# Optimization experiments

Measured on AMD Instinct MI355X. Metric: run time of the kernel, lower is better.

The kernel has to match this reference:

```python
import jax, jax.numpy as jnp
import numpy as np
import math

HEAD_DIM = 32
N_Q_HEADS = 32
N_KV_HEADS = 8
ROPE_BASE = 10000.0
NEG_INF = -1e9


def _rope_cos_sin(seq_len, dtype):
    inv_freq = 1.0 / (ROPE_BASE ** (jnp.arange(0, HEAD_DIM, 2, dtype=jnp.float32) / HEAD_DIM))
    pos = jnp.arange(seq_len, dtype=jnp.float32)
    freqs = pos[:, None] * inv_freq[None, :]          # [S, D/2]
    emb = jnp.concatenate([freqs, freqs], axis=-1)     # [S, D]
    return jnp.cos(emb).astype(dtype), jnp.sin(emb).astype(dtype)


def _rotate_half(x):
    x1, x2 = jnp.split(x, 2, axis=-1)
    return jnp.concatenate([-x2, x1], axis=-1)


def _apply_rope(x, cos, sin):
    # x: [B, H, S, D]; cos/sin: [S, D]
    return x * cos[None, None] + _rotate_half(x) * sin[None, None]


def setup_inputs() -> dict:
    key = jax.random.key(0)
    ks = jax.random.split(key, 5)
    B, S, D = 2, 2048, 1024
    sc = 1.0 / math.sqrt(D)
    return {
        "hidden_states": jax.random.normal(ks[0], (B, S, D), jnp.float32),
        "attention_mask": jnp.ones((B, S), jnp.int32),
        "Wq": jax.random.normal(ks[1], (1024, 1024), jnp.float32) * sc,
        "Wk": jax.random.normal(ks[2], (256, 1024), jnp.float32) * sc,
        "Wv": jax.random.normal(ks[3], (256, 1024), jnp.float32) * sc,
        "Wo": jax.random.normal(ks[4], (1024, 1024), jnp.float32) * sc,
    }


def reference(hidden_states, attention_mask, Wq, Wk, Wv, Wo):
    B, S, D = hidden_states.shape
    group = N_Q_HEADS // N_KV_HEADS

    q = (hidden_states @ Wq.T).reshape(B, S, N_Q_HEADS, HEAD_DIM).transpose(0, 2, 1, 3)
    k = (hidden_states @ Wk.T).reshape(B, S, N_KV_HEADS, HEAD_DIM).transpose(0, 2, 1, 3)
    v = (hidden_states @ Wv.T).reshape(B, S, N_KV_HEADS, HEAD_DIM).transpose(0, 2, 1, 3)

    cos, sin = _rope_cos_sin(S, q.dtype)
    q = _apply_rope(q, cos, sin)
    k = _apply_rope(k, cos, sin)

    k = jnp.repeat(k, group, axis=1)  # [B, 32, S, D]
    v = jnp.repeat(v, group, axis=1)

    scores = jnp.einsum("bhqd,bhkd->bhqk", q, k) / math.sqrt(HEAD_DIM)

    causal = jnp.tril(jnp.ones((S, S), bool))
    allowed = causal[None, None] & (attention_mask[:, None, None, :] != 0)
    scores = jnp.where(allowed, scores, NEG_INF)

    attn = jax.nn.softmax(scores, axis=-1)
    out = jnp.einsum("bhqk,bhkd->bhqd", attn, v)  # [B, 32, S, 32]
    out = out.transpose(0, 2, 1, 3).reshape(B, S, D)
    return out @ Wo.T
```

## Files before the change

kernel.cpp:

```cpp
#include <hip/hip_runtime.h>

typedef __bf16 bf16x8 __attribute__((ext_vector_type(8)));
typedef __bf16 bf16x4 __attribute__((ext_vector_type(4)));
typedef short short4v __attribute__((ext_vector_type(4)));
typedef float f32x4 __attribute__((ext_vector_type(4)));

__device__ __forceinline__ f32x4 mfma16(bf16x8 a, bf16x8 b, f32x4 c) {
  return __builtin_amdgcn_mfma_f32_16x16x32_bf16(a, b, c, 0, 0, 0);
}

__device__ __forceinline__ f32x4 mfma16k16(bf16x4 a, bf16x4 b, f32x4 c) {
#if __has_builtin(__builtin_amdgcn_mfma_f32_16x16x16bf16_1k)
  short4v as = __builtin_bit_cast(short4v, a);
  short4v bs = __builtin_bit_cast(short4v, b);
  return __builtin_amdgcn_mfma_f32_16x16x16bf16_1k(as, bs, c, 0, 0, 0);
#else
  f32x4 d;
  asm volatile("v_mfma_f32_16x16x16_bf16 %0, %1, %2, %3"
               : "=v"(d)
               : "v"(a), "v"(b), "v"(c));
  return d;
#endif
}

__device__ __forceinline__ float fast_exp2(float x) {
  return __builtin_amdgcn_exp2f(x);
}

typedef const __attribute__((address_space(1))) void gvoid_t;
typedef __attribute__((address_space(3))) void svoid_t;
__device__ __forceinline__ void lds16(const __bf16* g, __bf16* l) {
  __builtin_amdgcn_global_load_lds((gvoid_t*)g, (svoid_t*)l, 16, 0, 0);
}

__global__ __launch_bounds__(256) void prep(const float* __restrict__ hidden,
                                            const float* __restrict__ Wq,
                                            const float* __restrict__ Wk,
                                            const float* __restrict__ Wv,
                                            const float* __restrict__ Wo,
                                            __bf16* __restrict__ hb,
                                            __bf16* __restrict__ Wqkvb,
                                            __bf16* __restrict__ Wob) {
  int q = blockIdx.x * 256 + threadIdx.x;
  const float* src;
  __bf16* dst;
  if (q < 1048576) {
    src = hidden; dst = hb;
  } else if ((q -= 1048576) < 262144) {
    src = Wq; dst = Wqkvb;
  } else if ((q -= 262144) < 65536) {
    src = Wk; dst = Wqkvb + 1048576;
  } else if ((q -= 65536) < 65536) {
    src = Wv; dst = Wqkvb + 1310720;
  } else {
    q -= 65536;
    src = Wo; dst = Wob;
  }
  float4 v = *(const float4*)(src + (size_t)q * 4);
  bf16x4 o = { (__bf16)v.x, (__bf16)v.y, (__bf16)v.z, (__bf16)v.w };
  *(bf16x4*)(dst + (size_t)q * 4) = o;
}

template <bool BF16_OUT>
__global__ __launch_bounds__(256) void gemm_nt(const __bf16* __restrict__ A,
                                               const __bf16* __restrict__ B,
                                               void* __restrict__ Cv, int N) {
  __shared__ __bf16 As[2][128][32];
  __shared__ __bf16 Bs[2][128][32];
  const int m0 = blockIdx.x * 128, n0 = blockIdx.y * 128;
  const int tid = threadIdx.x;
  const int wave = tid >> 6, lane = tid & 63, quad = lane >> 4, l16 = lane & 15;
  const int wr = wave >> 1, wc = wave & 1;
  const int srow = 32 * wave;
  const __bf16* Ag = A + (size_t)(m0 + srow + (lane >> 2)) * 1024 + (lane & 3) * 8;
  const __bf16* Bg = B + (size_t)(n0 + srow + (lane >> 2)) * 1024 + (lane & 3) * 8;
  f32x4 acc[4][4] = {};

  auto stage = [&](int buf, int k0) {
    lds16(Ag + k0, &As[buf][srow][0]);
    lds16(Ag + 16 * 1024 + k0, &As[buf][srow + 16][0]);
    lds16(Bg + k0, &Bs[buf][srow][0]);
    lds16(Bg + 16 * 1024 + k0, &Bs[buf][srow + 16][0]);
  };
  stage(0, 0);
  __syncthreads();
  int buf = 0;
  for (int k0 = 0; k0 < 1024; k0 += 32) {
    if (k0 + 32 < 1024) stage(buf ^ 1, k0 + 32);
    bf16x8 af[4], bfr[4];
#pragma unroll
    for (int i = 0; i < 4; i++)
      af[i] = *(bf16x8*)&As[buf][64 * wr + 16 * i + l16][quad * 8];
#pragma unroll
    for (int j = 0; j < 4; j++)
      bfr[j] = *(bf16x8*)&Bs[buf][64 * wc + 16 * j + l16][quad * 8];
#pragma unroll
    for (int i = 0; i < 4; i++)
#pragma unroll
      for (int j = 0; j < 4; j++) acc[i][j] = mfma16(af[i], bfr[j], acc[i][j]);
    __syncthreads();
    buf ^= 1;
  }
#pragma unroll
  for (int i = 0; i < 4; i++)
#pragma unroll
    for (int j = 0; j < 4; j++)
#pragma unroll
      for (int r = 0; r < 4; r++) {
        int row = m0 + 64 * wr + 16 * i + quad * 4 + r;
        int col = n0 + 64 * wc + 16 * j + l16;
        if constexpr (BF16_OUT)
          ((__bf16*)Cv)[(size_t)row * N + col] = (__bf16)acc[i][j][r];
        else
          ((float*)Cv)[(size_t)row * N + col] = acc[i][j][r];
      }
}

__global__ __launch_bounds__(256) void ropevt(__bf16* __restrict__ QKV,
                                              __bf16* __restrict__ VT,
                                              const int* __restrict__ amask,
                                              float* __restrict__ maskb) {
  int idx = blockIdx.x * 256 + threadIdx.x;
  if (idx < 2621440) {
    __bf16* base;
    int m, i;
    if (idx < 2097152) {
      m = idx >> 9;
      int h = (idx >> 4) & 31;
      i = idx & 15;
      base = QKV + (size_t)m * 1536 + h * 32;
    } else {
      int j = idx - 2097152;
      m = j >> 7;
      int h = (j >> 4) & 7;
      i = j & 15;
      base = QKV + (size_t)m * 1536 + 1024 + h * 32;
    }
    int s = m & 2047;
    float inv = __expf(-(float)i * 0.5756462732485114f);
    float ang = (float)s * inv;
    float sn, cs;
    __sincosf(ang, &sn, &cs);
    float x0 = (float)base[i];
    float x1 = (float)base[i + 16];
    base[i] = (__bf16)(x0 * cs - x1 * sn);
    base[i + 16] = (__bf16)(x1 * cs + x0 * sn);
  } else {
    int j = idx - 2621440;
    if (j < 4096) maskb[j] = amask[j] ? -16.0f : -1.5e9f;
    int s4 = j & 511;
    int d = (j >> 9) & 31;
    int hb_ = j >> 14;
    int s = s4 * 4;
    int b_ = hb_ >> 3, hkv_ = hb_ & 7;
    const __bf16* src = QKV + (size_t)(b_ * 2048 + s) * 1536 + 1280 + hkv_ * 32 + d;
    bf16x4 ov = { src[0], src[1536], src[3072], src[4608] };
    *(bf16x4*)&VT[((size_t)hb_ * 32 + d) * 2048 + s] = ov;
  }
}

__global__ __launch_bounds__(256, 4) void attn(const __bf16* __restrict__ QKV,
                                               const __bf16* __restrict__ VT,
                                               const float* __restrict__ maskb,
                                               float* __restrict__ Opart,
                                               float* __restrict__ rspart) {
  __shared__ __bf16 Ks[2][64][40];
  __shared__ __bf16 Vs[2][32][72];
  const int tid = threadIdx.x;
  const int wave = tid >> 6, lane = tid & 63;
  const int quad = lane >> 4, l16 = lane & 15;
  const int b = blockIdx.z, h = blockIdx.y, hkv = h >> 2;
  const int xp = blockIdx.x >> 1, z = blockIdx.x & 1;
  const float SC2 = 0.25503472f;

  const int sk_key = tid >> 2, sk_ch = (tid & 3) * 8;
  const int sv_d = tid >> 3, sv_seg = (tid & 7) * 8;
  const __bf16* ksrc = QKV + (size_t)(b * 2048 + sk_key) * 1536 + 1024 + hkv * 32 + sk_ch;
  const __bf16* vsrc = VT + ((size_t)(b * 8 + hkv) * 32 + sv_d) * 2048 + sv_seg;
  const float* mrow = maskb + b * 2048;

  for (int sp = 0; sp < 2; sp++) {
    const int strip = sp ? 15 - xp : xp;
    const int t_begin = z ? (strip + 1) : 0;
    const int t_end = z ? (2 * strip + 2) : (strip + 1);
    const int qw = strip * 128 + wave * 32;
    const int q_row0 = qw + l16, q_row1 = qw + 16 + l16;
    const __bf16* qbase = QKV + (size_t)(b * 2048 + qw + l16) * 1536 + h * 32 + quad * 8;
    bf16x8 qf0 = *(const bf16x8*)qbase;
    bf16x8 qf1 = *(const bf16x8*)(qbase + 16 * 1536);

    {
      uint4 kr = *(const uint4*)(ksrc + (size_t)t_begin * 64 * 1536);
      uint4 vr = *(const uint4*)(vsrc + (size_t)t_begin * 64);
      *(uint4*)&Ks[0][sk_key][sk_ch] = kr;
      *(uint4*)&Vs[0][sv_d][sv_seg] = vr;
    }
    __syncthreads();

    f32x4 o00 = {}, o01 = {}, o10 = {}, o11 = {};
    float rs0 = 0.f, rs1 = 0.f;
    int buf = 0;

    for (int t = t_begin; t < t_end; t++) {
      const int kv0 = t << 6;
      const bool more = (t + 1 < t_end);
      uint4 kr, vr;
      if (more) {
        kr = *(const uint4*)(ksrc + (size_t)(t + 1) * 64 * 1536);
        vr = *(const uint4*)(vsrc + (size_t)(t + 1) * 64);
      }
      if (kv0 <= qw + 31) {
        bf16x8 kf[4];
#pragma unroll
        for (int kt = 0; kt < 4; kt++)
          kf[kt] = *(bf16x8*)&Ks[buf][16 * kt + l16][quad * 8];
        f32x4 s0[4], s1[4];
#pragma unroll
        for (int kt = 0; kt < 4; kt++) {
          f32x4 zz = {};
          s0[kt] = mfma16(kf[kt], qf0, zz);
          s1[kt] = mfma16(kf[kt], qf1, zz);
        }
        bf16x4 pb0[4], pb1[4];
        if (kv0 + 63 <= qw) {
#pragma unroll
          for (int kt = 0; kt < 4; kt++) {
            const int kb = kv0 + 16 * kt + 4 * quad;
            float4 mb = *(const float4*)(mrow + kb);
#pragma unroll
            for (int r = 0; r < 4; r++) {
              float e0 = fast_exp2(fmaf(s0[kt][r], SC2, (&mb.x)[r]));
              float e1 = fast_exp2(fmaf(s1[kt][r], SC2, (&mb.x)[r]));
              rs0 += e0;
              rs1 += e1;
              pb0[kt][r] = (__bf16)e0;
              pb1[kt][r] = (__bf16)e1;
            }
          }
        } else {
#pragma unroll
          for (int kt = 0; kt < 4; kt++) {
            const int kb = kv0 + 16 * kt + 4 * quad;
            float4 mb = *(const float4*)(mrow + kb);
#pragma unroll
            for (int r = 0; r < 4; r++) {
              const int key = kb + r;
              float e0 = fast_exp2(fmaf(s0[kt][r], SC2, (&mb.x)[r]));
              float e1 = fast_exp2(fmaf(s1[kt][r], SC2, (&mb.x)[r]));
              e0 = (key <= q_row0) ? e0 : 0.f;
              e1 = (key <= q_row1) ? e1 : 0.f;
              rs0 += e0;
              rs1 += e1;
              pb0[kt][r] = (__bf16)e0;
              pb1[kt][r] = (__bf16)e1;
            }
          }
        }
#pragma unroll
        for (int kt = 0; kt < 4; kt++) {
          bf16x4 v0 = *(bf16x4*)&Vs[buf][l16][16 * kt + 4 * quad];
          bf16x4 v1 = *(bf16x4*)&Vs[buf][16 + l16][16 * kt + 4 * quad];
          o00 = mfma16k16(v0, pb0[kt], o00);
          o01 = mfma16k16(v1, pb0[kt], o01);
          o10 = mfma16k16(v0, pb1[kt], o10);
          o11 = mfma16k16(v1, pb1[kt], o11);
        }
      }
      if (more) {
        *(uint4*)&Ks[buf ^ 1][sk_key][sk_ch] = kr;
        *(uint4*)&Vs[buf ^ 1][sv_d][sv_seg] = vr;
      }
      __syncthreads();
      buf ^= 1;
    }
    rs0 += __shfl_xor(rs0, 16);
    rs0 += __shfl_xor(rs0, 32);
    rs1 += __shfl_xor(rs1, 16);
    rs1 += __shfl_xor(rs1, 32);
    float* Op = Opart + (size_t)z * 4096 * 1024;
    size_t row0 = (size_t)(b * 2048 + q_row0);
    size_t row1 = (size_t)(b * 2048 + q_row1);
    *(f32x4*)&Op[row0 * 1024 + h * 32 + quad * 4] = o00;
    *(f32x4*)&Op[row0 * 1024 + h * 32 + 16 + quad * 4] = o01;
    *(f32x4*)&Op[row1 * 1024 + h * 32 + quad * 4] = o10;
    *(f32x4*)&Op[row1 * 1024 + h * 32 + 16 + quad * 4] = o11;
    if (quad == 0) {
      size_t ri = ((size_t)(z * 2 + b) * 32 + h) * 2048;
      rspart[ri + q_row0] = rs0;
      rspart[ri + q_row1] = rs1;
    }
  }
}

__global__ __launch_bounds__(256) void combine(const float* __restrict__ Opart,
                                               const float* __restrict__ rspart,
                                               __bf16* __restrict__ Ob) {
  int idx = blockIdx.x * 256 + threadIdx.x;
  int row = idx >> 7, g = idx & 127;
  int b = row >> 11, q = row & 2047, h = g >> 2;
  size_t off = (size_t)row * 1024 + g * 8;
  float4 a0 = *(const float4*)(Opart + off);
  float4 a1 = *(const float4*)(Opart + off + 4);
  float4 c0 = *(const float4*)(Opart + 4194304 + off);
  float4 c1 = *(const float4*)(Opart + 4194304 + off + 4);
  size_t ri = ((size_t)b * 32 + h) * 2048 + q;
  float inv = 1.0f / (rspart[ri] + rspart[2 * 65536 + ri]);
  bf16x8 w = { (__bf16)((a0.x + c0.x) * inv), (__bf16)((a0.y + c0.y) * inv),
               (__bf16)((a0.z + c0.z) * inv), (__bf16)((a0.w + c0.w) * inv),
               (__bf16)((a1.x + c1.x) * inv), (__bf16)((a1.y + c1.y) * inv),
               (__bf16)((a1.z + c1.z) * inv), (__bf16)((a1.w + c1.w) * inv) };
  *(bf16x8*)&Ob[off] = w;
}

extern "C" void kernel_launch(void* const* d_in, const int* in_sizes, int n_in,
                              void* d_out, int out_size, void* d_ws, size_t ws_size,
                              hipStream_t stream) {
  const float* hidden = (const float*)d_in[0];
  const int* amask = (const int*)d_in[1];
  const float* Wq = (const float*)d_in[2];
  const float* Wk = (const float*)d_in[3];
  const float* Wv = (const float*)d_in[4];
  const float* Wo = (const float*)d_in[5];
  float* out = (float*)d_out;

  char* p = (char*)d_ws;
  auto carve = [&](size_t elems) {
    __bf16* r = (__bf16*)p;
    p += ((elems * 2 + 255) / 256) * 256;
    return r;
  };
  __bf16* hb = carve(4096ull * 1024);
  __bf16* Wqkvb = carve(1536ull * 1024);
  __bf16* Wob = carve(1024ull * 1024);
  __bf16* QKV = carve(4096ull * 1536);
  __bf16* VT = carve(4096ull * 256);
  __bf16* Ob = carve(4096ull * 1024);
  float* maskb = (float*)carve(8192);
  float* Opart = (float*)carve(2ull * 4096 * 1024 * 2);
  float* rspart = (float*)carve(2ull * 2 * 32 * 2048 * 2);

  prep<<<6656, 256, 0, stream>>>(hidden, Wq, Wk, Wv, Wo, hb, Wqkvb, Wob);

  gemm_nt<true><<<dim3(32, 12), 256, 0, stream>>>(hb, Wqkvb, QKV, 1536);

  ropevt<<<11264, 256, 0, stream>>>(QKV, VT, amask, maskb);

  attn<<<dim3(16, 32, 2), 256, 0, stream>>>(QKV, VT, maskb, Opart, rspart);

  combine<<<2048, 256, 0, stream>>>(Opart, rspart, Ob);

  gemm_nt<false><<<dim3(32, 8), 256, 0, stream>>>(Ob, Wob, (void*)out, 1024);
}
```

Baseline: 183.8 us.

## Fuse split-KV combine into output projection GEMM and store partials in bf16

Removes the separate combine kernel: the Wo GEMM now loads both attention partial outputs, sums them, scales by the inverse row-sum, and writes the bf16 A tile into shared memory itself. The attention kernel writes its partial outputs as bf16 instead of fp32, halving that write traffic and the intermediate Ob buffer is dropped. This saves a launch and a full read/write pass over the attention output, at the cost of register-staged A loads in the GEMM (no async lds path) and extra bf16 rounding of unnormalized partials.

```diff
diff --git a/kernel.cpp b/kernel.cpp
--- a/kernel.cpp
+++ b/kernel.cpp
@@ -61,10 +61,9 @@
   *(bf16x4*)(dst + (size_t)q * 4) = o;
 }
 
-template <bool BF16_OUT>
 __global__ __launch_bounds__(256) void gemm_nt(const __bf16* __restrict__ A,
                                                const __bf16* __restrict__ B,
-                                               void* __restrict__ Cv, int N) {
+                                               __bf16* __restrict__ Cv, int N) {
   __shared__ __bf16 As[2][128][32];
   __shared__ __bf16 Bs[2][128][32];
   const int m0 = blockIdx.x * 128, n0 = blockIdx.y * 128;
@@ -109,10 +108,96 @@
       for (int r = 0; r < 4; r++) {
         int row = m0 + 64 * wr + 16 * i + quad * 4 + r;
         int col = n0 + 64 * wc + 16 * j + l16;
-        if constexpr (BF16_OUT)
-          ((__bf16*)Cv)[(size_t)row * N + col] = (__bf16)acc[i][j][r];
-        else
-          ((float*)Cv)[(size_t)row * N + col] = acc[i][j][r];
+        Cv[(size_t)row * N + col] = (__bf16)acc[i][j][r];
+      }
+}
+
+__global__ __launch_bounds__(256) void gemm_wo(const __bf16* __restrict__ Op0,
+                                               const __bf16* __restrict__ Op1,
+                                               const float* __restrict__ rspart,
+                                               const __bf16* __restrict__ B,
+                                               float* __restrict__ C) {
+  __shared__ __bf16 As[2][128][32];
+  __shared__ __bf16 Bs[2][128][32];
+  const int m0 = blockIdx.x * 128, n0 = blockIdx.y * 128;
+  const int tid = threadIdx.x;
+  const int wave = tid >> 6, lane = tid & 63, quad = lane >> 4, l16 = lane & 15;
+  const int wr = wave >> 1, wc = wave & 1;
+  const int srow = 32 * wave;
+  const int r_in = srow + (lane >> 2), c_in = (lane & 3) * 8;
+  const int grow0 = m0 + r_in, grow1 = grow0 + 16;
+  const int b0 = grow0 >> 11, q0 = grow0 & 2047;
+  const int b1 = grow1 >> 11, q1 = grow1 & 2047;
+  const __bf16* Bg = B + (size_t)(n0 + r_in) * 1024 + c_in;
+  f32x4 acc[4][4] = {};
+
+  auto loadA = [&](int k0, bf16x8& a00, bf16x8& a01, bf16x8& a10, bf16x8& a11,
+                   float& i0, float& i1) {
+    const int h = k0 >> 5;
+    a00 = *(const bf16x8*)(Op0 + (size_t)grow0 * 1024 + k0 + c_in);
+    a01 = *(const bf16x8*)(Op1 + (size_t)grow0 * 1024 + k0 + c_in);
+    a10 = *(const bf16x8*)(Op0 + (size_t)grow1 * 1024 + k0 + c_in);
+    a11 = *(const bf16x8*)(Op1 + (size_t)grow1 * 1024 + k0 + c_in);
+    i0 = 1.0f / (rspart[((size_t)b0 * 32 + h) * 2048 + q0] +
+                 rspart[((size_t)(2 + b0) * 32 + h) * 2048 + q0]);
+    i1 = 1.0f / (rspart[((size_t)b1 * 32 + h) * 2048 + q1] +
+                 rspart[((size_t)(2 + b1) * 32 + h) * 2048 + q1]);
+  };
+  auto writeA = [&](int buf, bf16x8 a00, bf16x8 a01, bf16x8 a10, bf16x8 a11,
+                    float i0, float i1) {
+    bf16x8 w0, w1;
+#pragma unroll
+    for (int e = 0; e < 8; e++) {
+      w0[e] = (__bf16)(((float)a00[e] + (float)a01[e]) * i0);
+      w1[e] = (__bf16)(((float)a10[e] + (float)a11[e]) * i1);
+    }
+    *(bf16x8*)&As[buf][r_in][c_in] = w0;
+    *(bf16x8*)&As[buf][r_in + 16][c_in] = w1;
+  };
+
+  {
+    bf16x8 a00, a01, a10, a11;
+    float i0, i1;
+    loadA(0, a00, a01, a10, a11, i0, i1);
+    lds16(Bg, &Bs[0][srow][0]);
+    lds16(Bg + 16 * 1024, &Bs[0][srow + 16][0]);
+    writeA(0, a00, a01, a10, a11, i0, i1);
+  }
+  __syncthreads();
+  int buf = 0;
+  for (int k0 = 0; k0 < 1024; k0 += 32) {
+    const bool more = (k0 + 32) < 1024;
+    bf16x8 a00, a01, a10, a11;
+    float i0, i1;
+    if (more) {
+      loadA(k0 + 32, a00, a01, a10, a11, i0, i1);
+      lds16(Bg + k0 + 32, &Bs[buf ^ 1][srow][0]);
+      lds16(Bg + 16 * 1024 + k0 + 32, &Bs[buf ^ 1][srow + 16][0]);
+    }
+    bf16x8 af[4], bfr[4];
+#pragma unroll
+    for (int i = 0; i < 4; i++)
+      af[i] = *(bf16x8*)&As[buf][64 * wr + 16 * i + l16][quad * 8];
+#pragma unroll
+    for (int j = 0; j < 4; j++)
+      bfr[j] = *(bf16x8*)&Bs[buf][64 * wc + 16 * j + l16][quad * 8];
+#pragma unroll
+    for (int i = 0; i < 4; i++)
+#pragma unroll
+      for (int j = 0; j < 4; j++) acc[i][j] = mfma16(af[i], bfr[j], acc[i][j]);
+    if (more) writeA(buf ^ 1, a00, a01, a10, a11, i0, i1);
+    __syncthreads();
+    buf ^= 1;
+  }
+#pragma unroll
+  for (int i = 0; i < 4; i++)
+#pragma unroll
+    for (int j = 0; j < 4; j++)
+#pragma unroll
+      for (int r = 0; r < 4; r++) {
+        int row = m0 + 64 * wr + 16 * i + quad * 4 + r;
+        int col = n0 + 64 * wc + 16 * j + l16;
+        C[(size_t)row * 1024 + col] = acc[i][j][r];
       }
 }
 
@@ -162,7 +247,7 @@
 __global__ __launch_bounds__(256, 4) void attn(const __bf16* __restrict__ QKV,
                                                const __bf16* __restrict__ VT,
                                                const float* __restrict__ maskb,
-                                               float* __restrict__ Opart,
+                                               __bf16* __restrict__ Opart,
                                                float* __restrict__ rspart) {
   __shared__ __bf16 Ks[2][64][40];
   __shared__ __bf16 Vs[2][32][72];
@@ -277,39 +362,23 @@
     rs0 += __shfl_xor(rs0, 32);
     rs1 += __shfl_xor(rs1, 16);
     rs1 += __shfl_xor(rs1, 32);
-    float* Op = Opart + (size_t)z * 4096 * 1024;
+    __bf16* Op = Opart + (size_t)z * 4096 * 1024;
     size_t row0 = (size_t)(b * 2048 + q_row0);
     size_t row1 = (size_t)(b * 2048 + q_row1);
-    *(f32x4*)&Op[row0 * 1024 + h * 32 + quad * 4] = o00;
-    *(f32x4*)&Op[row0 * 1024 + h * 32 + 16 + quad * 4] = o01;
-    *(f32x4*)&Op[row1 * 1024 + h * 32 + quad * 4] = o10;
-    *(f32x4*)&Op[row1 * 1024 + h * 32 + 16 + quad * 4] = o11;
+    bf16x4 w00 = { (__bf16)o00[0], (__bf16)o00[1], (__bf16)o00[2], (__bf16)o00[3] };
+    bf16x4 w01 = { (__bf16)o01[0], (__bf16)o01[1], (__bf16)o01[2], (__bf16)o01[3] };
+    bf16x4 w10 = { (__bf16)o10[0], (__bf16)o10[1], (__bf16)o10[2], (__bf16)o10[3] };
+    bf16x4 w11 = { (__bf16)o11[0], (__bf16)o11[1], (__bf16)o11[2], (__bf16)o11[3] };
+    *(bf16x4*)&Op[row0 * 1024 + h * 32 + quad * 4] = w00;
+    *(bf16x4*)&Op[row0 * 1024 + h * 32 + 16 + quad * 4] = w01;
+    *(bf16x4*)&Op[row1 * 1024 + h * 32 + quad * 4] = w10;
+    *(bf16x4*)&Op[row1 * 1024 + h * 32 + 16 + quad * 4] = w11;
     if (quad == 0) {
       size_t ri = ((size_t)(z * 2 + b) * 32 + h) * 2048;
       rspart[ri + q_row0] = rs0;
       rspart[ri + q_row1] = rs1;
     }
   }
-}
-
-__global__ __launch_bounds__(256) void combine(const float* __restrict__ Opart,
-                                               const float* __restrict__ rspart,
-                                               __bf16* __restrict__ Ob) {
-  int idx = blockIdx.x * 256 + threadIdx.x;
-  int row = idx >> 7, g = idx & 127;
-  int b = row >> 11, q = row & 2047, h = g >> 2;
-  size_t off = (size_t)row * 1024 + g * 8;
-  float4 a0 = *(const float4*)(Opart + off);
-  float4 a1 = *(const float4*)(Opart + off + 4);
-  float4 c0 = *(const float4*)(Opart + 4194304 + off);
-  float4 c1 = *(const float4*)(Opart + 4194304 + off + 4);
-  size_t ri = ((size_t)b * 32 + h) * 2048 + q;
-  float inv = 1.0f / (rspart[ri] + rspart[2 * 65536 + ri]);
-  bf16x8 w = { (__bf16)((a0.x + c0.x) * inv), (__bf16)((a0.y + c0.y) * inv),
-               (__bf16)((a0.z + c0.z) * inv), (__bf16)((a0.w + c0.w) * inv),
-               (__bf16)((a1.x + c1.x) * inv), (__bf16)((a1.y + c1.y) * inv),
-               (__bf16)((a1.z + c1.z) * inv), (__bf16)((a1.w + c1.w) * inv) };
-  *(bf16x8*)&Ob[off] = w;
 }
 
 extern "C" void kernel_launch(void* const* d_in, const int* in_sizes, int n_in,
@@ -334,20 +403,18 @@
   __bf16* Wob = carve(1024ull * 1024);
   __bf16* QKV = carve(4096ull * 1536);
   __bf16* VT = carve(4096ull * 256);
-  __bf16* Ob = carve(4096ull * 1024);
   float* maskb = (float*)carve(8192);
-  float* Opart = (float*)carve(2ull * 4096 * 1024 * 2);
+  __bf16* Opart = carve(2ull * 4096 * 1024);
   float* rspart = (float*)carve(2ull * 2 * 32 * 2048 * 2);
 
   prep<<<6656, 256, 0, stream>>>(hidden, Wq, Wk, Wv, Wo, hb, Wqkvb, Wob);
 
-  gemm_nt<true><<<dim3(32, 12), 256, 0, stream>>>(hb, Wqkvb, QKV, 1536);
+  gemm_nt<<<dim3(32, 12), 256, 0, stream>>>(hb, Wqkvb, QKV, 1536);
 
   ropevt<<<11264, 256, 0, stream>>>(QKV, VT, amask, maskb);
 
   attn<<<dim3(16, 32, 2), 256, 0, stream>>>(QKV, VT, maskb, Opart, rspart);
 
-  combine<<<2048, 256, 0, stream>>>(Opart, rspart, Ob);
-
-  gemm_nt<false><<<dim3(32, 8), 256, 0, stream>>>(Ob, Wob, (void*)out, 1024);
-}
+  gemm_wo<<<dim3(32, 8), 256, 0, stream>>>(Opart, Opart + 4096ull * 1024,
+                                           rspart, Wob, out);
+}
```

New measurement: 195.4 us. 6.3% more time.
